# Kernel optimization log

Measured on AMD Instinct MI355X. Metric: run time of the kernel, lower is better.

## Reference

```python
import jax, jax.numpy as jnp
import numpy as np
import math

B, S, D = 4, 2048, 1024      # batch, seq, d_model
E, F_EXP = 16, 512           # n_experts_ffn, d_expert_ffn
N_SHARED, K_FFN = 2, 4       # shared experts, routed top-k
N_ROUTED = E - N_SHARED


def setup_inputs() -> dict:
    key = jax.random.key(0)
    k0, k1, k2, k3, k4 = jax.random.split(key, 5)
    token_stream = jax.random.normal(k0, (B, S, D), jnp.float32)
    selection_input = jax.random.normal(k1, (B, S, D), jnp.float32)
    # init per reset_parameters (std_scale = 1.0)
    keys_w = jax.random.normal(k2, (E, D, F_EXP), jnp.float32) / math.sqrt(D)
    values_w = jax.random.normal(k3, (E, F_EXP, D), jnp.float32) / math.sqrt(E * F_EXP)
    expert_sel = jax.random.normal(k4, (E, D), jnp.float32) / math.sqrt(D)
    bias_ffn = jnp.zeros((E,), jnp.float32)  # load-balancing bias buffer
    return {
        "token_stream": token_stream,
        "selection_input": selection_input,
        "keys_w": keys_w,
        "values_w": values_w,
        "expert_sel": expert_sel,
        "bias_ffn": bias_ffn,
    }


def reference(token_stream, selection_input, keys_w, values_w, expert_sel, bias_ffn):
    # ---- routing: sigmoid affinity over all experts ----
    affinity = jax.nn.sigmoid(jnp.einsum("bsd,ed->bse", selection_input, expert_sel))  # [B,S,E]
    # top-k over routed experts (bias only affects ranking, not gathered affinity)
    _, routed_idx = jax.lax.top_k(affinity[..., :N_ROUTED] + bias_ffn[:N_ROUTED], K_FFN)  # [B,S,k]
    shared_idx = jnp.broadcast_to(
        jnp.arange(N_ROUTED, E, dtype=routed_idx.dtype), routed_idx.shape[:-1] + (N_SHARED,)
    )
    sel = jnp.concatenate([routed_idx, shared_idx], axis=-1)  # [B,S,K], K = k + shared
    aff_sel = jnp.take_along_axis(affinity, sel, axis=-1)     # [B,S,K]

    # ---- expert FFN (cvmm = gather / grouped GEMM / weighted scatter) ----
    # dense per-expert key projection, then gather selected experts
    scores_all = jnp.einsum("bsd,edf->bsef", token_stream, keys_w)        # [B,S,E,f]
    scores = jnp.take_along_axis(scores_all, sel[..., None], axis=2)      # [B,S,K,f]
    scores = jax.nn.silu(scores)

    # combine: out = sum_k aff_k * (scores_k @ values[sel_k])
    onehot = jax.nn.one_hot(sel, E, dtype=scores.dtype)                   # [B,S,K,E]
    dispatch = jnp.einsum("bskf,bske->bsef", scores * aff_sel[..., None], onehot)  # [B,S,E,f]
    out = jnp.einsum("bsef,efd->bsd", dispatch, values_w)                 # [B,S,D]
    return out, sel
```

## Files before the change

kernel.cpp:

```cpp
#include <hip/hip_runtime.h>

typedef short short8 __attribute__((ext_vector_type(8)));
typedef float f32x4 __attribute__((ext_vector_type(4)));
typedef unsigned short u16;

#define TOK_N 8192
#define DMODEL 1024
#define NEXP 16
#define FEXP 512
#define NROUTED 14
#define KSEL 6
#define MAXTILES 400

__device__ __forceinline__ u16 f2bf(float f) {
  unsigned u = __float_as_uint(f);
  u += 0x7fff + ((u >> 16) & 1);
  return (u16)(u >> 16);
}

typedef const __attribute__((address_space(1))) unsigned int* gas_p;
typedef __attribute__((address_space(3))) unsigned int* las_p;
__device__ __forceinline__ void gload_lds16(const void* g, void* l) {
  __builtin_amdgcn_global_load_lds((gas_p)g, (las_p)l, 16, 0, 0);
}

__global__ void cast_bf16_k(const float* __restrict__ in, u16* __restrict__ out, int n8) {
  int i = blockIdx.x * blockDim.x + threadIdx.x;
  if (i >= n8) return;
  const float4* p = (const float4*)(in + (size_t)i * 8);
  float4 a = p[0], b = p[1];
  short8 v;
  v[0] = (short)f2bf(a.x); v[1] = (short)f2bf(a.y); v[2] = (short)f2bf(a.z); v[3] = (short)f2bf(a.w);
  v[4] = (short)f2bf(b.x); v[5] = (short)f2bf(b.y); v[6] = (short)f2bf(b.z); v[7] = (short)f2bf(b.w);
  *(short8*)(out + (size_t)i * 8) = v;
}

__global__ void transpose_cast_k(const float* __restrict__ in, u16* __restrict__ out, int R, int C) {
  __shared__ u16 tile[32][33];
  int e = blockIdx.z;
  int c0 = blockIdx.x * 32, r0 = blockIdx.y * 32;
  int x = threadIdx.x, y = threadIdx.y;
  const float* ip = in + ((size_t)e * R + r0) * C + c0;
  #pragma unroll
  for (int i = 0; i < 4; i++)
    tile[y + 8 * i][x] = f2bf(ip[(size_t)(y + 8 * i) * C + x]);
  __syncthreads();
  u16* op = out + ((size_t)e * C + c0) * R + r0;
  #pragma unroll
  for (int i = 0; i < 4; i++)
    op[(size_t)(y + 8 * i) * R + x] = tile[x][y + 8 * i];
}

__global__ void routing_k(const float* __restrict__ selin, const float* __restrict__ esel,
                          const float* __restrict__ bias, float* __restrict__ out_sel,
                          unsigned* __restrict__ sel_pack, float* __restrict__ aff6) {
  int tok = blockIdx.x;
  int t = threadIdx.x;
  int e = t & 15, chunk = t >> 4;
  const float4* r4 = (const float4*)(selin + (size_t)tok * DMODEL + chunk * 64);
  const float4* w4 = (const float4*)(esel + (size_t)e * DMODEL + chunk * 64);
  float p = 0.f;
  #pragma unroll
  for (int i = 0; i < 16; i++) {
    float4 a = r4[i], b = w4[i];
    p += a.x * b.x + a.y * b.y + a.z * b.z + a.w * b.w;
  }
  __shared__ float part[16][17];
  __shared__ float aff[16];
  __shared__ float lbias[NROUTED];
  if (t < NROUTED) lbias[t] = bias[t];
  part[chunk][e] = p;
  __syncthreads();
  if (t < 16) {
    float s = 0.f;
    #pragma unroll
    for (int c = 0; c < 16; c++) s += part[c][t];
    aff[t] = 1.f / (1.f + expf(-s));
  }
  __syncthreads();
  if (t == 0) {
    unsigned pack = 0;
    unsigned taken = 0;
    #pragma unroll
    for (int k = 0; k < 4; k++) {
      float best = -3.4e38f; int bi = 0;
      for (int q = 0; q < NROUTED; q++) {
        if (taken & (1u << q)) continue;
        float v = aff[q] + lbias[q];
        if (v > best) { best = v; bi = q; }
      }
      taken |= 1u << bi;
      pack |= (unsigned)bi << (4 * k);
      out_sel[(size_t)tok * KSEL + k] = (float)bi;
      aff6[(size_t)tok * KSEL + k] = aff[bi];
    }
    pack |= 14u << 16; pack |= 15u << 20;
    out_sel[(size_t)tok * KSEL + 4] = 14.f;
    out_sel[(size_t)tok * KSEL + 5] = 15.f;
    aff6[(size_t)tok * KSEL + 4] = aff[14];
    aff6[(size_t)tok * KSEL + 5] = aff[15];
    sel_pack[tok] = pack;
  }
}

__global__ void scatter_k(const unsigned* __restrict__ sel_pack, const float* __restrict__ aff6,
                          int* __restrict__ counts, int* __restrict__ tokk,
                          float* __restrict__ affl) {
  __shared__ int lcnt[16], lbase[16], lcur[16];
  int t = threadIdx.x;
  int tok = blockIdx.x * 256 + t;
  if (t < 16) lcnt[t] = 0;
  __syncthreads();
  unsigned pack = sel_pack[tok];
  int eid[KSEL];
  #pragma unroll
  for (int k = 0; k < KSEL; k++) {
    eid[k] = (pack >> (4 * k)) & 15;
    atomicAdd(&lcnt[eid[k]], 1);
  }
  __syncthreads();
  if (t < 16) {
    lbase[t] = atomicAdd(&counts[t * 16], lcnt[t]);
    lcur[t] = 0;
  }
  __syncthreads();
  #pragma unroll
  for (int k = 0; k < KSEL; k++) {
    int e = eid[k];
    int slot = lbase[e] + atomicAdd(&lcur[e], 1);
    tokk[e * TOK_N + slot] = tok * 8 + k;
    affl[e * TOK_N + slot] = aff6[(size_t)tok * KSEL + k];
  }
}

__global__ void tilelist_k(const int* __restrict__ counts, int* __restrict__ tiles,
                           int* __restrict__ ntiles, int* __restrict__ pbase) {
  __shared__ int tc[16], pb[16];
  int t = threadIdx.x;
  if (t < 16) tc[t] = (counts[t * 16] + 127) >> 7;
  __syncthreads();
  if (t == 0) {
    int s = 0;
    for (int e = 0; e < 16; e++) { pb[e] = s; s += tc[e]; }
    *ntiles = s;
    int s2 = 0;
    for (int e = 0; e < 16; e++) { pbase[e] = s2; s2 += counts[e * 16]; }
  }
  __syncthreads();
  if (t < 16) {
    int b = pb[t], n = tc[t];
    for (int i = 0; i < n; i++) tiles[b + i] = t | (i << 8);
  }
}

template<int AK, int PASS, int NY>
__global__ __launch_bounds__(256, 2) void moe_gemm_k(
    const u16* __restrict__ Abase, const u16* __restrict__ Bbase,
    const int* __restrict__ counts, const int* __restrict__ tokk,
    const float* __restrict__ affl, const int* __restrict__ tiles,
    const int* __restrict__ ntiles, const int* __restrict__ pbase,
    u16* __restrict__ scores_out, float* __restrict__ out) {
  int p = blockIdx.x;
  int slot = (p & 7) + 8 * (p / (8 * NY));
  int y = (p >> 3) % NY;
  if (slot >= *ntiles) return;
  int desc = tiles[slot];
  int e = desc & 15;
  int m0 = (desc >> 8) << 7;
  int cnt = counts[e * 16];
  int pbe = pbase[e];
  int n0 = y * 128;
  int t = threadIdx.x;
  int lane = t & 63, w = t >> 6;
  int wr = w >> 1, wc = w & 1;

  __shared__ u16 Al[2][128][64];
  __shared__ u16 Bl[2][128][64];

  const int* tl = tokk + e * TOK_N + m0;
  const float* al = affl + e * TOK_N + m0;
  const u16* Bp = Bbase + (size_t)e * 524288;

  f32x4 acc[4][4];
  #pragma unroll
  for (int m = 0; m < 4; m++)
    #pragma unroll
    for (int n = 0; n < 4; n++)
      acc[m][n] = (f32x4){0.f, 0.f, 0.f, 0.f};

  int jj = lane & 7, rl = lane >> 3;
  const u16* ag[4]; const u16* bg[4];
  #pragma unroll
  for (int r = 0; r < 4; r++) {
    int row = r * 32 + w * 8 + rl;
    int lr = (m0 + row < cnt) ? row : 0;
    int ar;
    if (PASS == 2) {
      int tk = tl[lr];
      ar = tk >> 3;
    } else {
      ar = pbe + m0 + lr;
    }
    int cs = (jj ^ (row & 7)) * 8;
    ag[r] = Abase + (size_t)ar * AK + cs;
    bg[r] = Bp + (size_t)(n0 + row) * AK + cs;
  }

#define STAGE(B, K0)                                             \
  _Pragma("unroll")                                              \
  for (int r = 0; r < 4; r++) {                                  \
    gload_lds16(ag[r] + (K0), &Al[B][r * 32 + w * 8][0]);        \
    gload_lds16(bg[r] + (K0), &Bl[B][r * 32 + w * 8][0]);        \
  }

#define COMPUTE(B)                                                         \
  _Pragma("unroll")                                                        \
  for (int kk = 0; kk < 2; kk++) {                                         \
    int lc = kk * 4 + (lane >> 4);                                         \
    short8 af[4], bf[4];                                                   \
    _Pragma("unroll")                                                      \
    for (int m = 0; m < 4; m++) {                                          \
      int row = wr * 64 + m * 16 + (lane & 15);                            \
      af[m] = *(const short8*)&Al[B][row][(lc ^ (row & 7)) * 8];           \
    }                                                                      \
    _Pragma("unroll")                                                      \
    for (int n = 0; n < 4; n++) {                                          \
      int row = wc * 64 + n * 16 + (lane & 15);                            \
      bf[n] = *(const short8*)&Bl[B][row][(lc ^ (row & 7)) * 8];           \
    }                                                                      \
    _Pragma("unroll")                                                      \
    for (int m = 0; m < 4; m++)                                            \
      _Pragma("unroll")                                                    \
      for (int n = 0; n < 4; n++)                                          \
        acc[m][n] = __builtin_amdgcn_mfma_f32_16x16x32_bf16(af[m], bf[n],  \
                                                            acc[m][n], 0, 0, 0); \
  }

#define VWAIT8 asm volatile("s_waitcnt vmcnt(8)" ::: "memory")
#define VWAIT0 asm volatile("s_waitcnt vmcnt(0)" ::: "memory")
#define BARR  __builtin_amdgcn_s_barrier()
#define PIN   __builtin_amdgcn_sched_barrier(0)

  constexpr int NIT = AK / 64;
  STAGE(0, 0)
  #pragma unroll 1
  for (int it = 0; it < NIT - 2; it += 2) {
    STAGE(1, (it + 1) * 64)
    VWAIT8; BARR; PIN;
    COMPUTE(0)
    BARR; PIN;
    STAGE(0, (it + 2) * 64)
    VWAIT8; BARR; PIN;
    COMPUTE(1)
    BARR; PIN;
  }
  STAGE(1, (NIT - 1) * 64)
  VWAIT8; BARR; PIN;
  COMPUTE(0)
  BARR; PIN;
  VWAIT0; BARR; PIN;
  COMPUTE(1)

#undef STAGE
#undef COMPUTE
#undef VWAIT8
#undef VWAIT0
#undef BARR
#undef PIN

  int cbase = n0 + wc * 64 + (lane & 15);
  #pragma unroll
  for (int m = 0; m < 4; m++) {
    int rbase = wr * 64 + m * 16 + ((lane >> 4) << 2);
    #pragma unroll
    for (int q = 0; q < 4; q++) {
      int row = rbase + q;
      if (m0 + row >= cnt) continue;
      if (PASS == 2) {
        float aff = al[row];
        size_t base = (size_t)(pbe + m0 + row) * FEXP;
        #pragma unroll
        for (int n = 0; n < 4; n++) {
          float v = acc[m][n][q];
          float s = aff * v / (1.f + expf(-v));
          scores_out[base + cbase + n * 16] = f2bf(s);
        }
      } else {
        int tk = tl[row];
        size_t base = (size_t)(tk >> 3) * DMODEL;
        #pragma unroll
        for (int n = 0; n < 4; n++)
          atomicAdd(&out[base + cbase + n * 16], acc[m][n][q]);
      }
    }
  }
}

extern "C" void kernel_launch(void* const* d_in, const int* in_sizes, int n_in,
                              void* d_out, int out_size, void* d_ws, size_t ws_size,
                              hipStream_t stream) {
  (void)in_sizes; (void)n_in; (void)out_size; (void)ws_size;
  const float* token_stream    = (const float*)d_in[0];
  const float* selection_input = (const float*)d_in[1];
  const float* keys_w          = (const float*)d_in[2];
  const float* values_w        = (const float*)d_in[3];
  const float* expert_sel      = (const float*)d_in[4];
  const float* bias_ffn        = (const float*)d_in[5];

  float* out     = (float*)d_out;
  float* out_sel = out + (size_t)TOK_N * DMODEL;

  char* ws = (char*)d_ws;
  u16*      Xbf      = (u16*)(ws + 0);
  u16*      keysT    = (u16*)(ws + 16777216);
  u16*      valuesT  = (u16*)(ws + 33554432);
  u16*      scoresbf = (u16*)(ws + 50331648);
  int*      counts   = (int*)(ws + 100663296);
  int*      tokk     = (int*)(ws + 100664320);
  float*    affl     = (float*)(ws + 101188608);
  unsigned* sel_pack = (unsigned*)(ws + 101712896);
  float*    aff6     = (float*)(ws + 101745664);
  int*      tiles    = (int*)(ws + 101942272);
  int*      ntiles   = (int*)(ws + 101946368);
  int*      pbase    = (int*)(ws + 101946432);

  hipMemsetAsync(out, 0, (size_t)TOK_N * DMODEL * sizeof(float), stream);
  hipMemsetAsync(counts, 0, 1024, stream);

  cast_bf16_k<<<4096, 256, 0, stream>>>(token_stream, Xbf, TOK_N * DMODEL / 8);
  transpose_cast_k<<<dim3(16, 32, 16), dim3(32, 8), 0, stream>>>(keys_w, keysT, 1024, 512);
  transpose_cast_k<<<dim3(32, 16, 16), dim3(32, 8), 0, stream>>>(values_w, valuesT, 512, 1024);

  routing_k<<<TOK_N, 256, 0, stream>>>(selection_input, expert_sel, bias_ffn,
                                       out_sel, sel_pack, aff6);
  scatter_k<<<TOK_N / 256, 256, 0, stream>>>(sel_pack, aff6, counts, tokk, affl);
  tilelist_k<<<1, 64, 0, stream>>>(counts, tiles, ntiles, pbase);

  moe_gemm_k<1024, 2, 4><<<MAXTILES * 4, 256, 0, stream>>>(Xbf, keysT, counts, tokk, affl,
                                                           tiles, ntiles, pbase,
                                                           scoresbf, nullptr);
  moe_gemm_k<512, 3, 8><<<MAXTILES * 8, 256, 0, stream>>>(scoresbf, valuesT, counts, tokk, affl,
                                                          tiles, ntiles, pbase,
                                                          nullptr, out);
}
```

Baseline: 416.0 us.

## Widen MoE GEMM tiles to 128x256 with 8 waves and XCD-grouped slots

Both grouped GEMM passes now use 512-thread blocks, each computing a 128x256 output tile instead of 128x128, so every A tile is loaded half as often per output column. The LDS staging is reorganised to match: 2 A rows and 4 B rows are loaded per thread per stage, and the vmcnt wait is adjusted. Blocks are remapped so that each XCD handles a contiguous range of tile slots, with all column blocks of a tile on the same XCD, to improve L2 reuse of expert weights and A rows. In exchange, the ~96KB of LDS limits each CU to one block, which removes cross-block latency hiding and adds a risk of load imbalance across XCDs.

```diff
diff --git a/kernel.cpp b/kernel.cpp
--- a/kernel.cpp
+++ b/kernel.cpp
@@ -154,28 +154,30 @@
 }
 
 template<int AK, int PASS, int NY>
-__global__ __launch_bounds__(256, 2) void moe_gemm_k(
+__global__ __launch_bounds__(512, 1) void moe_gemm_k(
     const u16* __restrict__ Abase, const u16* __restrict__ Bbase,
     const int* __restrict__ counts, const int* __restrict__ tokk,
     const float* __restrict__ affl, const int* __restrict__ tiles,
     const int* __restrict__ ntiles, const int* __restrict__ pbase,
     u16* __restrict__ scores_out, float* __restrict__ out) {
   int p = blockIdx.x;
-  int slot = (p & 7) + 8 * (p / (8 * NY));
-  int y = (p >> 3) % NY;
+  int xcd = p & 7;
+  int i = p >> 3;
+  int slot = xcd * (MAXTILES / 8) + i / NY;
+  int y = i % NY;
   if (slot >= *ntiles) return;
   int desc = tiles[slot];
   int e = desc & 15;
   int m0 = (desc >> 8) << 7;
   int cnt = counts[e * 16];
   int pbe = pbase[e];
-  int n0 = y * 128;
+  int n0 = y * 256;
   int t = threadIdx.x;
   int lane = t & 63, w = t >> 6;
-  int wr = w >> 1, wc = w & 1;
+  int wr = w >> 2, wc = w & 3;
 
   __shared__ u16 Al[2][128][64];
-  __shared__ u16 Bl[2][128][64];
+  __shared__ u16 Bl[2][256][64];
 
   const int* tl = tokk + e * TOK_N + m0;
   const float* al = affl + e * TOK_N + m0;
@@ -189,10 +191,11 @@
       acc[m][n] = (f32x4){0.f, 0.f, 0.f, 0.f};
 
   int jj = lane & 7, rl = lane >> 3;
-  const u16* ag[4]; const u16* bg[4];
-  #pragma unroll
-  for (int r = 0; r < 4; r++) {
-    int row = r * 32 + w * 8 + rl;
+  int cs = (jj ^ rl) * 8;
+  const u16* ag[2]; const u16* bg[4];
+  #pragma unroll
+  for (int r = 0; r < 2; r++) {
+    int row = w * 16 + r * 8 + rl;
     int lr = (m0 + row < cnt) ? row : 0;
     int ar;
     if (PASS == 2) {
@@ -201,17 +204,21 @@
     } else {
       ar = pbe + m0 + lr;
     }
-    int cs = (jj ^ (row & 7)) * 8;
     ag[r] = Abase + (size_t)ar * AK + cs;
+  }
+  #pragma unroll
+  for (int r = 0; r < 4; r++) {
+    int row = w * 32 + r * 8 + rl;
     bg[r] = Bp + (size_t)(n0 + row) * AK + cs;
   }
 
 #define STAGE(B, K0)                                             \
   _Pragma("unroll")                                              \
-  for (int r = 0; r < 4; r++) {                                  \
-    gload_lds16(ag[r] + (K0), &Al[B][r * 32 + w * 8][0]);        \
-    gload_lds16(bg[r] + (K0), &Bl[B][r * 32 + w * 8][0]);        \
-  }
+  for (int r = 0; r < 2; r++)                                    \
+    gload_lds16(ag[r] + (K0), &Al[B][w * 16 + r * 8][0]);        \
+  _Pragma("unroll")                                              \
+  for (int r = 0; r < 4; r++)                                    \
+    gload_lds16(bg[r] + (K0), &Bl[B][w * 32 + r * 8][0]);
 
 #define COMPUTE(B)                                                         \
   _Pragma("unroll")                                                        \
@@ -236,7 +243,7 @@
                                                             acc[m][n], 0, 0, 0); \
   }
 
-#define VWAIT8 asm volatile("s_waitcnt vmcnt(8)" ::: "memory")
+#define VWAIT6 asm volatile("s_waitcnt vmcnt(6)" ::: "memory")
 #define VWAIT0 asm volatile("s_waitcnt vmcnt(0)" ::: "memory")
 #define BARR  __builtin_amdgcn_s_barrier()
 #define PIN   __builtin_amdgcn_sched_barrier(0)
@@ -246,16 +253,16 @@
   #pragma unroll 1
   for (int it = 0; it < NIT - 2; it += 2) {
     STAGE(1, (it + 1) * 64)
-    VWAIT8; BARR; PIN;
+    VWAIT6; BARR; PIN;
     COMPUTE(0)
     BARR; PIN;
     STAGE(0, (it + 2) * 64)
-    VWAIT8; BARR; PIN;
+    VWAIT6; BARR; PIN;
     COMPUTE(1)
     BARR; PIN;
   }
   STAGE(1, (NIT - 1) * 64)
-  VWAIT8; BARR; PIN;
+  VWAIT6; BARR; PIN;
   COMPUTE(0)
   BARR; PIN;
   VWAIT0; BARR; PIN;
@@ -263,7 +270,7 @@
 
 #undef STAGE
 #undef COMPUTE
-#undef VWAIT8
+#undef VWAIT6
 #undef VWAIT0
 #undef BARR
 #undef PIN
@@ -336,10 +343,10 @@
   scatter_k<<<TOK_N / 256, 256, 0, stream>>>(sel_pack, aff6, counts, tokk, affl);
   tilelist_k<<<1, 64, 0, stream>>>(counts, tiles, ntiles, pbase);
 
-  moe_gemm_k<1024, 2, 4><<<MAXTILES * 4, 256, 0, stream>>>(Xbf, keysT, counts, tokk, affl,
+  moe_gemm_k<1024, 2, 2><<<MAXTILES * 2, 512, 0, stream>>>(Xbf, keysT, counts, tokk, affl,
                                                            tiles, ntiles, pbase,
                                                            scoresbf, nullptr);
-  moe_gemm_k<512, 3, 8><<<MAXTILES * 8, 256, 0, stream>>>(scoresbf, valuesT, counts, tokk, affl,
+  moe_gemm_k<512, 3, 4><<<MAXTILES * 4, 512, 0, stream>>>(scoresbf, valuesT, counts, tokk, affl,
                                                           tiles, ntiles, pbase,
                                                           nullptr, out);
 }
```

Result: slower. 442.6 us (+6.4%).
